# Performance work log

Hardware: AMD Instinct MI355X
Metric: run time of the kernel (lower is better)

The kernel has to match this reference:

```python
import jax, jax.numpy as jnp
import numpy as np
from jax import lax

B = 8192
H = 64      # hidden_size
O = 3       # output_size (== LSTM input size)
L = 2       # num_layers


def setup_inputs() -> dict:
    key = jax.random.key(0)
    ks = jax.random.split(key, 16)
    s = 1.0 / np.sqrt(H)
    inp = {
        "x": jax.random.normal(ks[0], (B, 1, O), dtype=jnp.float32),
        "hidden": jax.random.normal(ks[1], (L, B, H), dtype=jnp.float32),
        "cell": jax.random.normal(ks[2], (L, B, H), dtype=jnp.float32),
        # layer 0 LSTM params (PyTorch gate order i, f, g, o)
        "Wih0": jax.random.uniform(ks[3], (4 * H, O), jnp.float32, -s, s),
        "Whh0": jax.random.uniform(ks[4], (4 * H, H), jnp.float32, -s, s),
        "bih0": jax.random.uniform(ks[5], (4 * H,), jnp.float32, -s, s),
        "bhh0": jax.random.uniform(ks[6], (4 * H,), jnp.float32, -s, s),
        # layer 1 LSTM params
        "Wih1": jax.random.uniform(ks[7], (4 * H, H), jnp.float32, -s, s),
        "Whh1": jax.random.uniform(ks[8], (4 * H, H), jnp.float32, -s, s),
        "bih1": jax.random.uniform(ks[9], (4 * H,), jnp.float32, -s, s),
        "bhh1": jax.random.uniform(ks[10], (4 * H,), jnp.float32, -s, s),
        # output projection
        "Wfc": jax.random.uniform(ks[11], (O, H), jnp.float32, -s, s),
        "bfc": jax.random.uniform(ks[12], (O,), jnp.float32, -s, s),
        "num_steps": 64,
    }
    return inp


def _lstm_layer_step(x_t, h, c, Wih, Whh, b):
    # x_t: [B, in], h/c: [B, H]; gates in PyTorch order i, f, g, o
    gates = x_t @ Wih.T + h @ Whh.T + b  # [B, 4H]
    i, f, g, o = jnp.split(gates, 4, axis=-1)
    c_new = jax.nn.sigmoid(f) * c + jax.nn.sigmoid(i) * jnp.tanh(g)
    h_new = jax.nn.sigmoid(o) * jnp.tanh(c_new)
    return h_new, c_new


def reference(x, hidden, cell, Wih0, Whh0, bih0, bhh0,
              Wih1, Whh1, bih1, bhh1, Wfc, bfc, num_steps):
    layers = ((Wih0, Whh0, bih0 + bhh0), (Wih1, Whh1, bih1 + bhh1))

    def step(carry, _):
        inp, h, c = carry  # inp: [B, O], h/c: [L, B, H]
        x_t = inp
        hs, cs = [], []
        for l, (Wih, Whh, b) in enumerate(layers):
            h_l, c_l = _lstm_layer_step(x_t, h[l], c[l], Wih, Whh, b)
            hs.append(h_l)
            cs.append(c_l)
            x_t = h_l
        out = x_t @ Wfc.T + bfc  # [B, O] -> fed back as next input
        return (out, jnp.stack(hs), jnp.stack(cs)), out

    init = (x[:, 0, :], hidden, cell)
    _, outs = lax.scan(step, init, None, length=num_steps)  # [T, B, O]
    return jnp.transpose(outs, (1, 0, 2))  # [B, T, O]
```

## Files before the change

kernel.cpp:

```cpp
#include <hip/hip_runtime.h>

typedef __attribute__((ext_vector_type(8))) short v8s;
typedef __attribute__((ext_vector_type(4))) float v4f;

#define NB 16
#define TMAX 64
#define B_TOT 8192

#define BL0_U 0
#define BL1_U 32768
#define BFC_U 98304
#define NUSH  100352
#define B0_F  50176
#define B1_F  50432
#define BFC3_F 50688

__device__ __forceinline__ unsigned short f2bh(float f) {
    unsigned u = __float_as_uint(f);
    return (unsigned short)((u + 0x7fffu + ((u >> 16) & 1u)) >> 16);
}
__device__ __forceinline__ float bh2f(unsigned short h) {
    return __uint_as_float(((unsigned)h) << 16);
}
__device__ __forceinline__ float sigm(float x) {
    return 1.f / (1.f + __expf(-x));
}
__device__ __forceinline__ float tanh_(float x) {
    float e = __expf(-2.f * fabsf(x));
    float r = (1.f - e) / (1.f + e);
    return copysignf(r, x);
}
__device__ __forceinline__ v8s ldfrag(const unsigned short* p) { return *(const v8s*)p; }

#define MFMA(a, b, c) __builtin_amdgcn_mfma_f32_16x16x32_bf16((a), (b), (c), 0, 0, 0)

__global__ void repack(const float* __restrict__ Whh0,
                       const float* __restrict__ bih0, const float* __restrict__ bhh0,
                       const float* __restrict__ Wih1, const float* __restrict__ Whh1,
                       const float* __restrict__ bih1, const float* __restrict__ bhh1,
                       const float* __restrict__ Wfc,  const float* __restrict__ bfc,
                       float* __restrict__ wsf) {
    unsigned idx = blockIdx.x * 256 + threadIdx.x;
    unsigned short* wsu = (unsigned short*)wsf;
    if (idx < NUSH) {
        unsigned u, fid, l, e, s, kst, n, r, k;
        float wv;
        if (idx < BL1_U) {
            u = idx; fid = u >> 9; l = (u >> 3) & 63; e = u & 7;
            s = fid & 1; unsigned t = fid >> 1; kst = t & 1; n = t >> 1;
            r = n * 16 + (l & 15); k = kst * 32 + ((l >> 4) * 8) + e;
            wv = Whh0[r * 64 + k];
        } else if (idx < BFC_U) {
            u = idx - BL1_U; fid = u >> 9; l = (u >> 3) & 63; e = u & 7;
            s = fid & 1; unsigned t = fid >> 1; kst = t & 3; n = t >> 2;
            r = n * 16 + (l & 15); k = kst * 32 + ((l >> 4) * 8) + e;
            wv = (k < 64) ? Wih1[r * 64 + k] : Whh1[r * 64 + (k - 64)];
        } else {
            u = idx - BFC_U; fid = u >> 9; l = (u >> 3) & 63; e = u & 7;
            s = fid & 1; kst = fid >> 1;
            unsigned o = l & 15; k = kst * 32 + ((l >> 4) * 8) + e;
            wv = (o < 3) ? Wfc[o * 64 + k] : 0.f;
        }
        unsigned short hi = f2bh(wv);
        wsu[idx] = s ? f2bh(wv - bh2f(hi)) : hi;
    } else {
        unsigned jj = idx - NUSH;
        if (jj < 256) wsf[B0_F + jj] = bih0[jj] + bhh0[jj];
        else if (jj < 512) wsf[B1_F + (jj - 256)] = bih1[jj - 256] + bhh1[jj - 256];
        else if (jj < 515) wsf[BFC3_F + (jj - 512)] = bfc[jj - 512];
    }
}

__global__ __launch_bounds__(256, 2) void lstm_main(
    const float* __restrict__ x0, const float* __restrict__ h_init,
    const float* __restrict__ c_init, const float* __restrict__ Wih0,
    const float* __restrict__ wsf, const int* __restrict__ nsp,
    float* __restrict__ out)
{
    __shared__ __align__(16) unsigned short Th0[2][2][2][512];
    __shared__ __align__(16) unsigned short Th1[2][2][2][512];
    __shared__ __align__(16) float xs[2][NB][4];
    __shared__ __align__(16) float obuf[NB][TMAX * 3];

    const unsigned short* wsu = (const unsigned short*)wsf;
    const int tid = threadIdx.x, l = tid & 63, w = tid >> 6;
    const int b0g = blockIdx.x * NB;
    const int n = nsp[0];
    const int j = w * 16 + (l & 15);
    const int jh = j >> 5, kl = j & 31;
    const int bfirst = (l >> 4) * 4;
    const int stoff = ((kl >> 3) * 128) + (kl & 7) + bfirst * 8;

    v8s bl0h[4][2], bl1h[4][4];
#pragma unroll
    for (int g = 0; g < 4; ++g) {
        const int n_ = 4 * g + w;
#pragma unroll
        for (int k = 0; k < 2; ++k)
            bl0h[g][k] = ldfrag(wsu + BL0_U + ((n_ * 2 + k) * 2 + 0) * 512 + l * 8);
#pragma unroll
        for (int k = 0; k < 4; ++k)
            bl1h[g][k] = ldfrag(wsu + BL1_U + ((n_ * 4 + k) * 2 + 0) * 512 + l * 8);
    }
    float bias0[4], bias1[4], wx[4][3];
#pragma unroll
    for (int g = 0; g < 4; ++g) {
        bias0[g] = wsf[B0_F + g * 64 + j];
        bias1[g] = wsf[B1_F + g * 64 + j];
#pragma unroll
        for (int oi = 0; oi < 3; ++oi) wx[g][oi] = Wih0[(g * 64 + j) * 3 + oi];
    }
    const float mybfc = ((l & 15) < 3) ? wsf[BFC3_F + (l & 15)] : 0.f;

    float c0[4], c1[4];
#pragma unroll
    for (int r = 0; r < 4; ++r) {
        const int b = bfirst + r, bg = b0g + b;
        c0[r] = c_init[bg * 64 + j];
        c1[r] = c_init[B_TOT * 64 + bg * 64 + j];
        float h0v = h_init[bg * 64 + j];
        float h1v = h_init[B_TOT * 64 + bg * 64 + j];
        unsigned short hh = f2bh(h0v);
        Th0[0][0][jh][stoff + r * 8] = hh;
        Th0[0][1][jh][stoff + r * 8] = f2bh(h0v - bh2f(hh));
        hh = f2bh(h1v);
        Th1[0][0][jh][stoff + r * 8] = hh;
        Th1[0][1][jh][stoff + r * 8] = f2bh(h1v - bh2f(hh));
    }
    if (tid < NB * 3) {
        int b = tid / 3, o = tid % 3;
        xs[0][b][o] = x0[(b0g + b) * 3 + o];
    }
    __syncthreads();

    int cur = 0;
    for (int t = 0; t < n; ++t) {
        const int nxt = cur ^ 1;
        v8s bl0l[4][2];
#pragma unroll
        for (int g = 0; g < 4; ++g)
#pragma unroll
            for (int k = 0; k < 2; ++k)
                bl0l[g][k] = ldfrag(wsu + BL0_U + (((4 * g + w) * 2 + k) * 2 + 1) * 512 + l * 8);

        v4f acc[4];
#pragma unroll
        for (int g = 0; g < 4; ++g) acc[g] = (v4f){bias0[g], bias0[g], bias0[g], bias0[g]};

#pragma unroll
        for (int r = 0; r < 4; ++r) {
            float4 xv = *(const float4*)&xs[cur][bfirst + r][0];
#pragma unroll
            for (int g = 0; g < 4; ++g)
                acc[g][r] += wx[g][0] * xv.x + wx[g][1] * xv.y + wx[g][2] * xv.z;
        }
#pragma unroll
        for (int k = 0; k < 2; ++k) {
            v8s ah = *(const v8s*)&Th0[cur][0][k][l * 8];
            v8s al = *(const v8s*)&Th0[cur][1][k][l * 8];
#pragma unroll
            for (int g = 0; g < 4; ++g) acc[g] = MFMA(ah, bl0h[g][k], acc[g]);
#pragma unroll
            for (int g = 0; g < 4; ++g) acc[g] = MFMA(al, bl0h[g][k], acc[g]);
#pragma unroll
            for (int g = 0; g < 4; ++g) acc[g] = MFMA(ah, bl0l[g][k], acc[g]);
        }
#pragma unroll
        for (int r = 0; r < 4; ++r) {
            float ig = sigm(acc[0][r]), fg = sigm(acc[1][r]);
            float gg = tanh_(acc[2][r]), og = sigm(acc[3][r]);
            float cn = fg * c0[r] + ig * gg;
            c0[r] = cn;
            float h = og * tanh_(cn);
            unsigned short hh = f2bh(h);
            Th0[nxt][0][jh][stoff + r * 8] = hh;
            Th0[nxt][1][jh][stoff + r * 8] = f2bh(h - bh2f(hh));
        }
        v8s bl1l[4][4];
#pragma unroll
        for (int g = 0; g < 4; ++g)
#pragma unroll
            for (int k = 0; k < 4; ++k)
                bl1l[g][k] = ldfrag(wsu + BL1_U + (((4 * g + w) * 4 + k) * 2 + 1) * 512 + l * 8);

        __syncthreads();

#pragma unroll
        for (int g = 0; g < 4; ++g) acc[g] = (v4f){bias1[g], bias1[g], bias1[g], bias1[g]};
#pragma unroll
        for (int k = 0; k < 4; ++k) {
            v8s ah, al;
            if (k < 2) { ah = *(const v8s*)&Th0[nxt][0][k][l * 8];
                         al = *(const v8s*)&Th0[nxt][1][k][l * 8]; }
            else       { ah = *(const v8s*)&Th1[cur][0][k - 2][l * 8];
                         al = *(const v8s*)&Th1[cur][1][k - 2][l * 8]; }
#pragma unroll
            for (int g = 0; g < 4; ++g) acc[g] = MFMA(ah, bl1h[g][k], acc[g]);
#pragma unroll
            for (int g = 0; g < 4; ++g) acc[g] = MFMA(al, bl1h[g][k], acc[g]);
#pragma unroll
            for (int g = 0; g < 4; ++g) acc[g] = MFMA(ah, bl1l[g][k], acc[g]);
        }
#pragma unroll
        for (int r = 0; r < 4; ++r) {
            float ig = sigm(acc[0][r]), fg = sigm(acc[1][r]);
            float gg = tanh_(acc[2][r]), og = sigm(acc[3][r]);
            float cn = fg * c1[r] + ig * gg;
            c1[r] = cn;
            float h = og * tanh_(cn);
            unsigned short hh = f2bh(h);
            Th1[nxt][0][jh][stoff + r * 8] = hh;
            Th1[nxt][1][jh][stoff + r * 8] = f2bh(h - bh2f(hh));
        }
        __syncthreads();

        if (w == 0) {
            v8s bfh[2], bfl[2];
#pragma unroll
            for (int k = 0; k < 2; ++k) {
                bfh[k] = ldfrag(wsu + BFC_U + (k * 2 + 0) * 512 + l * 8);
                bfl[k] = ldfrag(wsu + BFC_U + (k * 2 + 1) * 512 + l * 8);
            }
            v4f af = (v4f){mybfc, mybfc, mybfc, mybfc};
#pragma unroll
            for (int k = 0; k < 2; ++k) {
                v8s ah = *(const v8s*)&Th1[nxt][0][k][l * 8];
                v8s al = *(const v8s*)&Th1[nxt][1][k][l * 8];
                af = MFMA(ah, bfh[k], af);
                af = MFMA(al, bfh[k], af);
                af = MFMA(ah, bfl[k], af);
            }
            if ((l & 15) < 3) {
                const int o = l & 15;
#pragma unroll
                for (int r = 0; r < 4; ++r) {
                    const int b = bfirst + r;
                    float v = af[r];
                    obuf[b][t * 3 + o] = v;
                    xs[nxt][b][o] = v;
                }
            }
        }
        __syncthreads();
        cur = nxt;
    }

    const int tot = NB * n * 3;
    for (int i = tid; i < tot; i += 256) {
        int b = i / (n * 3), r2 = i % (n * 3);
        out[(b0g + b) * (n * 3) + r2] = obuf[b][r2];
    }
}

extern "C" void kernel_launch(void* const* d_in, const int* in_sizes, int n_in,
                              void* d_out, int out_size, void* d_ws, size_t ws_size,
                              hipStream_t stream) {
    const float* x    = (const float*)d_in[0];
    const float* hid  = (const float*)d_in[1];
    const float* cel  = (const float*)d_in[2];
    const float* Wih0 = (const float*)d_in[3];
    const float* Whh0 = (const float*)d_in[4];
    const float* bih0 = (const float*)d_in[5];
    const float* bhh0 = (const float*)d_in[6];
    const float* Wih1 = (const float*)d_in[7];
    const float* Whh1 = (const float*)d_in[8];
    const float* bih1 = (const float*)d_in[9];
    const float* bhh1 = (const float*)d_in[10];
    const float* Wfc  = (const float*)d_in[11];
    const float* bfc  = (const float*)d_in[12];
    const int*   nst  = (const int*)d_in[13];
    float* ws  = (float*)d_ws;
    float* outp = (float*)d_out;

    const int repack_threads = NUSH + 515;
    repack<<<(repack_threads + 255) / 256, 256, 0, stream>>>(
        Whh0, bih0, bhh0, Wih1, Whh1, bih1, bhh1, Wfc, bfc, ws);
    lstm_main<<<B_TOT / NB, 256, 0, stream>>>(x, hid, cel, Wih0, ws, nst, outp);
}
```

Baseline: 399.6 us.

## Split gate columns across 8 waves with LDS gate exchange for activations

```diff
diff --git a/kernel.cpp b/kernel.cpp
--- a/kernel.cpp
+++ b/kernel.cpp
@@ -6,6 +6,7 @@
 #define NB 16
 #define TMAX 64
 #define B_TOT 8192
+#define GP 21
 
 #define BL0_U 0
 #define BL1_U 32768
@@ -71,7 +72,8 @@
     }
 }
 
-__global__ __launch_bounds__(256, 2) void lstm_main(
+__global__ __launch_bounds__(512) __attribute__((amdgpu_waves_per_eu(4)))
+void lstm_main(
     const float* __restrict__ x0, const float* __restrict__ h_init,
     const float* __restrict__ c_init, const float* __restrict__ Wih0,
     const float* __restrict__ wsf, const int* __restrict__ nsp,
@@ -79,6 +81,7 @@
 {
     __shared__ __align__(16) unsigned short Th0[2][2][2][512];
     __shared__ __align__(16) unsigned short Th1[2][2][2][512];
+    __shared__ float gbuf[256][GP];
     __shared__ __align__(16) float xs[2][NB][4];
     __shared__ __align__(16) float obuf[NB][TMAX * 3];
 
@@ -86,46 +89,51 @@
     const int tid = threadIdx.x, l = tid & 63, w = tid >> 6;
     const int b0g = blockIdx.x * NB;
     const int n = nsp[0];
-    const int j = w * 16 + (l & 15);
-    const int jh = j >> 5, kl = j & 31;
+    const int n0 = 2 * w;
+    const int colA = n0 * 16 + (l & 15);
     const int bfirst = (l >> 4) * 4;
-    const int stoff = ((kl >> 3) * 128) + (kl & 7) + bfirst * 8;
-
-    v8s bl0h[4][2], bl1h[4][4];
-#pragma unroll
-    for (int g = 0; g < 4; ++g) {
-        const int n_ = 4 * g + w;
-#pragma unroll
-        for (int k = 0; k < 2; ++k)
-            bl0h[g][k] = ldfrag(wsu + BL0_U + ((n_ * 2 + k) * 2 + 0) * 512 + l * 8);
-#pragma unroll
-        for (int k = 0; k < 4; ++k)
-            bl1h[g][k] = ldfrag(wsu + BL1_U + ((n_ * 4 + k) * 2 + 0) * 512 + l * 8);
-    }
-    float bias0[4], bias1[4], wx[4][3];
-#pragma unroll
-    for (int g = 0; g < 4; ++g) {
-        bias0[g] = wsf[B0_F + g * 64 + j];
-        bias1[g] = wsf[B1_F + g * 64 + j];
-#pragma unroll
-        for (int oi = 0; oi < 3; ++oi) wx[g][oi] = Wih0[(g * 64 + j) * 3 + oi];
+    const int ab = tid >> 5;
+    const int aj0 = (tid & 31) << 1;
+
+    v8s b0h[2][2], b1hA[2][2];
+#pragma unroll
+    for (int nt = 0; nt < 2; ++nt) {
+#pragma unroll
+        for (int k = 0; k < 2; ++k) {
+            b0h[nt][k]  = ldfrag(wsu + BL0_U + ((((n0 + nt) * 2 + k) * 2 + 0) << 9) + (l << 3));
+            b1hA[nt][k] = ldfrag(wsu + BL1_U + ((((n0 + nt) * 4 + k) * 2 + 0) << 9) + (l << 3));
+        }
+    }
+    float bias0[2], bias1[2], wx[2][3];
+#pragma unroll
+    for (int nt = 0; nt < 2; ++nt) {
+        const int cc = colA + nt * 16;
+        bias0[nt] = wsf[B0_F + cc];
+        bias1[nt] = wsf[B1_F + cc];
+#pragma unroll
+        for (int oi = 0; oi < 3; ++oi) wx[nt][oi] = Wih0[cc * 3 + oi];
     }
     const float mybfc = ((l & 15) < 3) ? wsf[BFC3_F + (l & 15)] : 0.f;
 
-    float c0[4], c1[4];
-#pragma unroll
-    for (int r = 0; r < 4; ++r) {
-        const int b = bfirst + r, bg = b0g + b;
-        c0[r] = c_init[bg * 64 + j];
-        c1[r] = c_init[B_TOT * 64 + bg * 64 + j];
-        float h0v = h_init[bg * 64 + j];
-        float h1v = h_init[B_TOT * 64 + bg * 64 + j];
-        unsigned short hh = f2bh(h0v);
-        Th0[0][0][jh][stoff + r * 8] = hh;
-        Th0[0][1][jh][stoff + r * 8] = f2bh(h0v - bh2f(hh));
-        hh = f2bh(h1v);
-        Th1[0][0][jh][stoff + r * 8] = hh;
-        Th1[0][1][jh][stoff + r * 8] = f2bh(h1v - bh2f(hh));
+    float c0[2], c1[2];
+    {
+        const int bg = b0g + ab;
+#pragma unroll
+        for (int m = 0; m < 2; ++m) {
+            const int jj = aj0 + m;
+            c0[m] = c_init[bg * 64 + jj];
+            c1[m] = c_init[B_TOT * 64 + bg * 64 + jj];
+            float h0v = h_init[bg * 64 + jj];
+            float h1v = h_init[B_TOT * 64 + bg * 64 + jj];
+            const int jh = jj >> 5, kl = jj & 31;
+            const int idx = ((kl >> 3) << 7) + (ab << 3) + (kl & 7);
+            unsigned short hh = f2bh(h0v);
+            Th0[0][0][jh][idx] = hh;
+            Th0[0][1][jh][idx] = f2bh(h0v - bh2f(hh));
+            hh = f2bh(h1v);
+            Th1[0][0][jh][idx] = hh;
+            Th1[0][1][jh][idx] = f2bh(h1v - bh2f(hh));
+        }
     }
     if (tid < NB * 3) {
         int b = tid / 3, o = tid % 3;
@@ -136,91 +144,164 @@
     int cur = 0;
     for (int t = 0; t < n; ++t) {
         const int nxt = cur ^ 1;
-        v8s bl0l[4][2];
-#pragma unroll
-        for (int g = 0; g < 4; ++g)
+        v8s b0l[2][2];
+#pragma unroll
+        for (int nt = 0; nt < 2; ++nt)
 #pragma unroll
             for (int k = 0; k < 2; ++k)
-                bl0l[g][k] = ldfrag(wsu + BL0_U + (((4 * g + w) * 2 + k) * 2 + 1) * 512 + l * 8);
-
-        v4f acc[4];
-#pragma unroll
-        for (int g = 0; g < 4; ++g) acc[g] = (v4f){bias0[g], bias0[g], bias0[g], bias0[g]};
-
-#pragma unroll
-        for (int r = 0; r < 4; ++r) {
-            float4 xv = *(const float4*)&xs[cur][bfirst + r][0];
-#pragma unroll
-            for (int g = 0; g < 4; ++g)
-                acc[g][r] += wx[g][0] * xv.x + wx[g][1] * xv.y + wx[g][2] * xv.z;
-        }
-#pragma unroll
-        for (int k = 0; k < 2; ++k) {
-            v8s ah = *(const v8s*)&Th0[cur][0][k][l * 8];
-            v8s al = *(const v8s*)&Th0[cur][1][k][l * 8];
-#pragma unroll
-            for (int g = 0; g < 4; ++g) acc[g] = MFMA(ah, bl0h[g][k], acc[g]);
-#pragma unroll
-            for (int g = 0; g < 4; ++g) acc[g] = MFMA(al, bl0h[g][k], acc[g]);
-#pragma unroll
-            for (int g = 0; g < 4; ++g) acc[g] = MFMA(ah, bl0l[g][k], acc[g]);
-        }
-#pragma unroll
-        for (int r = 0; r < 4; ++r) {
-            float ig = sigm(acc[0][r]), fg = sigm(acc[1][r]);
-            float gg = tanh_(acc[2][r]), og = sigm(acc[3][r]);
-            float cn = fg * c0[r] + ig * gg;
-            c0[r] = cn;
+                b0l[nt][k] = ldfrag(wsu + BL0_U + ((((n0 + nt) * 2 + k) * 2 + 1) << 9) + (l << 3));
+
+        {
+            v4f acc[2];
+#pragma unroll
+            for (int nt = 0; nt < 2; ++nt)
+                acc[nt] = (v4f){bias0[nt], bias0[nt], bias0[nt], bias0[nt]};
+#pragma unroll
+            for (int r = 0; r < 4; ++r) {
+                float4 xv = *(const float4*)&xs[cur][bfirst + r][0];
+#pragma unroll
+                for (int nt = 0; nt < 2; ++nt)
+                    acc[nt][r] += wx[nt][0] * xv.x + wx[nt][1] * xv.y + wx[nt][2] * xv.z;
+            }
+#pragma unroll
+            for (int k = 0; k < 2; ++k) {
+                v8s ah = *(const v8s*)&Th0[cur][0][k][l * 8];
+                v8s al = *(const v8s*)&Th0[cur][1][k][l * 8];
+#pragma unroll
+                for (int nt = 0; nt < 2; ++nt) {
+                    acc[nt] = MFMA(ah, b0h[nt][k], acc[nt]);
+                    acc[nt] = MFMA(al, b0h[nt][k], acc[nt]);
+                    acc[nt] = MFMA(ah, b0l[nt][k], acc[nt]);
+                }
+            }
+#pragma unroll
+            for (int nt = 0; nt < 2; ++nt) {
+                const int cc = colA + nt * 16;
+#pragma unroll
+                for (int r = 0; r < 4; ++r) gbuf[cc][bfirst + r] = acc[nt][r];
+            }
+        }
+        __syncthreads();
+
+        v8s l01[2][2];
+#pragma unroll
+        for (int nt = 0; nt < 2; ++nt)
+#pragma unroll
+            for (int k = 0; k < 2; ++k)
+                l01[nt][k] = ldfrag(wsu + BL1_U + ((((n0 + nt) * 4 + k) * 2 + 1) << 9) + (l << 3));
+
+#pragma unroll
+        for (int m = 0; m < 2; ++m) {
+            const int jj = aj0 + m;
+            float ig = sigm(gbuf[jj][ab]);
+            float fg = sigm(gbuf[64 + jj][ab]);
+            float gg = tanh_(gbuf[128 + jj][ab]);
+            float og = sigm(gbuf[192 + jj][ab]);
+            float cn = fg * c0[m] + ig * gg;
+            c0[m] = cn;
             float h = og * tanh_(cn);
             unsigned short hh = f2bh(h);
-            Th0[nxt][0][jh][stoff + r * 8] = hh;
-            Th0[nxt][1][jh][stoff + r * 8] = f2bh(h - bh2f(hh));
-        }
-        v8s bl1l[4][4];
-#pragma unroll
-        for (int g = 0; g < 4; ++g)
-#pragma unroll
-            for (int k = 0; k < 4; ++k)
-                bl1l[g][k] = ldfrag(wsu + BL1_U + (((4 * g + w) * 4 + k) * 2 + 1) * 512 + l * 8);
-
-        __syncthreads();
-
-#pragma unroll
-        for (int g = 0; g < 4; ++g) acc[g] = (v4f){bias1[g], bias1[g], bias1[g], bias1[g]};
-#pragma unroll
-        for (int k = 0; k < 4; ++k) {
-            v8s ah, al;
-            if (k < 2) { ah = *(const v8s*)&Th0[nxt][0][k][l * 8];
-                         al = *(const v8s*)&Th0[nxt][1][k][l * 8]; }
-            else       { ah = *(const v8s*)&Th1[cur][0][k - 2][l * 8];
-                         al = *(const v8s*)&Th1[cur][1][k - 2][l * 8]; }
-#pragma unroll
-            for (int g = 0; g < 4; ++g) acc[g] = MFMA(ah, bl1h[g][k], acc[g]);
-#pragma unroll
-            for (int g = 0; g < 4; ++g) acc[g] = MFMA(al, bl1h[g][k], acc[g]);
-#pragma unroll
-            for (int g = 0; g < 4; ++g) acc[g] = MFMA(ah, bl1l[g][k], acc[g]);
-        }
-#pragma unroll
-        for (int r = 0; r < 4; ++r) {
-            float ig = sigm(acc[0][r]), fg = sigm(acc[1][r]);
-            float gg = tanh_(acc[2][r]), og = sigm(acc[3][r]);
-            float cn = fg * c1[r] + ig * gg;
-            c1[r] = cn;
+            const int jh = jj >> 5, kl = jj & 31;
+            const int idx = ((kl >> 3) << 7) + (ab << 3) + (kl & 7);
+            Th0[nxt][0][jh][idx] = hh;
+            Th0[nxt][1][jh][idx] = f2bh(h - bh2f(hh));
+        }
+        __syncthreads();
+
+        {
+            v4f acc[2];
+#pragma unroll
+            for (int nt = 0; nt < 2; ++nt)
+                acc[nt] = (v4f){bias1[nt], bias1[nt], bias1[nt], bias1[nt]};
+
+            v8s h2[2], l2[2];
+#pragma unroll
+            for (int nt = 0; nt < 2; ++nt) {
+                h2[nt] = ldfrag(wsu + BL1_U + ((((n0 + nt) * 4 + 2) * 2 + 0) << 9) + (l << 3));
+                l2[nt] = ldfrag(wsu + BL1_U + ((((n0 + nt) * 4 + 2) * 2 + 1) << 9) + (l << 3));
+            }
+            {
+                v8s ah = *(const v8s*)&Th0[nxt][0][0][l * 8];
+                v8s al = *(const v8s*)&Th0[nxt][1][0][l * 8];
+#pragma unroll
+                for (int nt = 0; nt < 2; ++nt) {
+                    acc[nt] = MFMA(ah, b1hA[nt][0], acc[nt]);
+                    acc[nt] = MFMA(al, b1hA[nt][0], acc[nt]);
+                    acc[nt] = MFMA(ah, l01[nt][0], acc[nt]);
+                }
+            }
+            v8s h3[2], l3[2];
+#pragma unroll
+            for (int nt = 0; nt < 2; ++nt) {
+                h3[nt] = ldfrag(wsu + BL1_U + ((((n0 + nt) * 4 + 3) * 2 + 0) << 9) + (l << 3));
+                l3[nt] = ldfrag(wsu + BL1_U + ((((n0 + nt) * 4 + 3) * 2 + 1) << 9) + (l << 3));
+            }
+            {
+                v8s ah = *(const v8s*)&Th0[nxt][0][1][l * 8];
+                v8s al = *(const v8s*)&Th0[nxt][1][1][l * 8];
+#pragma unroll
+                for (int nt = 0; nt < 2; ++nt) {
+                    acc[nt] = MFMA(ah, b1hA[nt][1], acc[nt]);
+                    acc[nt] = MFMA(al, b1hA[nt][1], acc[nt]);
+                    acc[nt] = MFMA(ah, l01[nt][1], acc[nt]);
+                }
+            }
+            {
+                v8s ah = *(const v8s*)&Th1[cur][0][0][l * 8];
+                v8s al = *(const v8s*)&Th1[cur][1][0][l * 8];
+#pragma unroll
+                for (int nt = 0; nt < 2; ++nt) {
+                    acc[nt] = MFMA(ah, h2[nt], acc[nt]);
+                    acc[nt] = MFMA(al, h2[nt], acc[nt]);
+                    acc[nt] = MFMA(ah, l2[nt], acc[nt]);
+                }
+            }
+            {
+                v8s ah = *(const v8s*)&Th1[cur][0][1][l * 8];
+                v8s al = *(const v8s*)&Th1[cur][1][1][l * 8];
+#pragma unroll
+                for (int nt = 0; nt < 2; ++nt) {
+                    acc[nt] = MFMA(ah, h3[nt], acc[nt]);
+                    acc[nt] = MFMA(al, h3[nt], acc[nt]);
+                    acc[nt] = MFMA(ah, l3[nt], acc[nt]);
+                }
+            }
+#pragma unroll
+            for (int nt = 0; nt < 2; ++nt) {
+                const int cc = colA + nt * 16;
+#pragma unroll
+                for (int r = 0; r < 4; ++r) gbuf[cc][bfirst + r] = acc[nt][r];
+            }
+        }
+        __syncthreads();
+
+        v8s bfh[2], bfl[2];
+        if (w == 0) {
+#pragma unroll
+            for (int k = 0; k < 2; ++k) {
+                bfh[k] = ldfrag(wsu + BFC_U + (((k) * 2 + 0) << 9) + (l << 3));
+                bfl[k] = ldfrag(wsu + BFC_U + (((k) * 2 + 1) << 9) + (l << 3));
+            }
+        }
+#pragma unroll
+        for (int m = 0; m < 2; ++m) {
+            const int jj = aj0 + m;
+            float ig = sigm(gbuf[jj][ab]);
+            float fg = sigm(gbuf[64 + jj][ab]);
+            float gg = tanh_(gbuf[128 + jj][ab]);
+            float og = sigm(gbuf[192 + jj][ab]);
+            float cn = fg * c1[m] + ig * gg;
+            c1[m] = cn;
             float h = og * tanh_(cn);
             unsigned short hh = f2bh(h);
-            Th1[nxt][0][jh][stoff + r * 8] = hh;
-            Th1[nxt][1][jh][stoff + r * 8] = f2bh(h - bh2f(hh));
+            const int jh = jj >> 5, kl = jj & 31;
+            const int idx = ((kl >> 3) << 7) + (ab << 3) + (kl & 7);
+            Th1[nxt][0][jh][idx] = hh;
+            Th1[nxt][1][jh][idx] = f2bh(h - bh2f(hh));
         }
         __syncthreads();
 
         if (w == 0) {
-            v8s bfh[2], bfl[2];
-#pragma unroll
-            for (int k = 0; k < 2; ++k) {
-                bfh[k] = ldfrag(wsu + BFC_U + (k * 2 + 0) * 512 + l * 8);
-                bfl[k] = ldfrag(wsu + BFC_U + (k * 2 + 1) * 512 + l * 8);
-            }
             v4f af = (v4f){mybfc, mybfc, mybfc, mybfc};
 #pragma unroll
             for (int k = 0; k < 2; ++k) {
@@ -246,7 +327,7 @@
     }
 
     const int tot = NB * n * 3;
-    for (int i = tid; i < tot; i += 256) {
+    for (int i = tid; i < tot; i += 512) {
         int b = i / (n * 3), r2 = i % (n * 3);
         out[(b0g + b) * (n * 3) + r2] = obuf[b][r2];
     }
@@ -275,5 +356,5 @@
     const int repack_threads = NUSH + 515;
     repack<<<(repack_threads + 255) / 256, 256, 0, stream>>>(
         Whh0, bih0, bhh0, Wih1, Whh1, bih1, bhh1, Wfc, bfc, ws);
-    lstm_main<<<B_TOT / NB, 256, 0, stream>>>(x, hid, cel, Wih0, ws, nst, outp);
-}
+    lstm_main<<<B_TOT / NB, 512, 0, stream>>>(x, hid, cel, Wih0, ws, nst, outp);
+}
```

Measured after the change: 697.8 us. +74.6%, slower.

## Switch LSTM recurrence to single fp16 MFMA and drop output LDS staging

Applied to the files above, without the earlier changes.

```diff
diff --git a/kernel.cpp b/kernel.cpp
--- a/kernel.cpp
+++ b/kernel.cpp
@@ -1,27 +1,19 @@
 #include <hip/hip_runtime.h>
 
-typedef __attribute__((ext_vector_type(8))) short v8s;
+typedef __attribute__((ext_vector_type(8))) _Float16 v8h;
 typedef __attribute__((ext_vector_type(4))) float v4f;
 
-#define NB 16
-#define TMAX 64
+#define MB 16
 #define B_TOT 8192
 
-#define BL0_U 0
-#define BL1_U 32768
-#define BFC_U 98304
-#define NUSH  100352
-#define B0_F  50176
-#define B1_F  50432
-#define BFC3_F 50688
-
-__device__ __forceinline__ unsigned short f2bh(float f) {
-    unsigned u = __float_as_uint(f);
-    return (unsigned short)((u + 0x7fffu + ((u >> 16) & 1u)) >> 16);
-}
-__device__ __forceinline__ float bh2f(unsigned short h) {
-    return __uint_as_float(((unsigned)h) << 16);
-}
+#define L0_H 0
+#define L1_H 16384
+#define FC_H 49152
+#define NHALF 50176
+#define B0_F 25088
+#define B1_F 25344
+#define BFC3_F 25600
+
 __device__ __forceinline__ float sigm(float x) {
     return 1.f / (1.f + __expf(-x));
 }
@@ -30,9 +22,8 @@
     float r = (1.f - e) / (1.f + e);
     return copysignf(r, x);
 }
-__device__ __forceinline__ v8s ldfrag(const unsigned short* p) { return *(const v8s*)p; }
-
-#define MFMA(a, b, c) __builtin_amdgcn_mfma_f32_16x16x32_bf16((a), (b), (c), 0, 0, 0)
+
+#define MFMAH(a, b, c) __builtin_amdgcn_mfma_f32_16x16x32_f16((a), (b), (c), 0, 0, 0)
 
 __global__ void repack(const float* __restrict__ Whh0,
                        const float* __restrict__ bih0, const float* __restrict__ bhh0,
@@ -41,214 +32,178 @@
                        const float* __restrict__ Wfc,  const float* __restrict__ bfc,
                        float* __restrict__ wsf) {
     unsigned idx = blockIdx.x * 256 + threadIdx.x;
-    unsigned short* wsu = (unsigned short*)wsf;
-    if (idx < NUSH) {
-        unsigned u, fid, l, e, s, kst, n, r, k;
+    _Float16* wsh = (_Float16*)wsf;
+    if (idx < NHALF) {
+        unsigned l = (idx >> 3) & 63, e = idx & 7;
         float wv;
-        if (idx < BL1_U) {
-            u = idx; fid = u >> 9; l = (u >> 3) & 63; e = u & 7;
-            s = fid & 1; unsigned t = fid >> 1; kst = t & 1; n = t >> 1;
-            r = n * 16 + (l & 15); k = kst * 32 + ((l >> 4) * 8) + e;
+        if (idx < L1_H) {
+            unsigned fid = idx >> 9, nt = fid >> 1, kst = fid & 1;
+            unsigned r = nt * 16 + (l & 15), k = kst * 32 + ((l >> 4) << 3) + e;
             wv = Whh0[r * 64 + k];
-        } else if (idx < BFC_U) {
-            u = idx - BL1_U; fid = u >> 9; l = (u >> 3) & 63; e = u & 7;
-            s = fid & 1; unsigned t = fid >> 1; kst = t & 3; n = t >> 2;
-            r = n * 16 + (l & 15); k = kst * 32 + ((l >> 4) * 8) + e;
+        } else if (idx < FC_H) {
+            unsigned u = idx - L1_H, fid = u >> 9, nt = fid >> 2, kst = fid & 3;
+            unsigned r = nt * 16 + (l & 15), k = kst * 32 + ((l >> 4) << 3) + e;
             wv = (k < 64) ? Wih1[r * 64 + k] : Whh1[r * 64 + (k - 64)];
         } else {
-            u = idx - BFC_U; fid = u >> 9; l = (u >> 3) & 63; e = u & 7;
-            s = fid & 1; kst = fid >> 1;
-            unsigned o = l & 15; k = kst * 32 + ((l >> 4) * 8) + e;
+            unsigned u = idx - FC_H, kst = u >> 9;
+            unsigned o = l & 15, k = kst * 32 + ((l >> 4) << 3) + e;
             wv = (o < 3) ? Wfc[o * 64 + k] : 0.f;
         }
-        unsigned short hi = f2bh(wv);
-        wsu[idx] = s ? f2bh(wv - bh2f(hi)) : hi;
+        wsh[idx] = (_Float16)wv;
     } else {
-        unsigned jj = idx - NUSH;
+        unsigned jj = idx - NHALF;
         if (jj < 256) wsf[B0_F + jj] = bih0[jj] + bhh0[jj];
         else if (jj < 512) wsf[B1_F + (jj - 256)] = bih1[jj - 256] + bhh1[jj - 256];
         else if (jj < 515) wsf[BFC3_F + (jj - 512)] = bfc[jj - 512];
     }
 }
 
-__global__ __launch_bounds__(256, 2) void lstm_main(
+__global__ __launch_bounds__(256)
+void lstm_main(
     const float* __restrict__ x0, const float* __restrict__ h_init,
     const float* __restrict__ c_init, const float* __restrict__ Wih0,
     const float* __restrict__ wsf, const int* __restrict__ nsp,
     float* __restrict__ out)
 {
-    __shared__ __align__(16) unsigned short Th0[2][2][2][512];
-    __shared__ __align__(16) unsigned short Th1[2][2][2][512];
-    __shared__ __align__(16) float xs[2][NB][4];
-    __shared__ __align__(16) float obuf[NB][TMAX * 3];
-
-    const unsigned short* wsu = (const unsigned short*)wsf;
+    __shared__ _Float16 Th0[2][2][512];
+    __shared__ _Float16 Th1[2][2][512];
+
+    const _Float16* wsh = (const _Float16*)wsf;
     const int tid = threadIdx.x, l = tid & 63, w = tid >> 6;
-    const int b0g = blockIdx.x * NB;
+    const int b0g = blockIdx.x * MB;
     const int n = nsp[0];
-    const int j = w * 16 + (l & 15);
-    const int jh = j >> 5, kl = j & 31;
+    const int c15 = l & 15;
     const int bfirst = (l >> 4) * 4;
-    const int stoff = ((kl >> 3) * 128) + (kl & 7) + bfirst * 8;
-
-    v8s bl0h[4][2], bl1h[4][4];
+    const int j = 16 * w + c15;
+    const int kh = j >> 5, kl = j & 31;
+    const int hwoff = ((kl >> 3) << 7) + (bfirst << 3) + (kl & 7);
+    const int sbase = l & 48;
+
+    v8h wb0[4][2], wb1[4][4], wfc2[2];
 #pragma unroll
     for (int g = 0; g < 4; ++g) {
-        const int n_ = 4 * g + w;
+        const int nt = 4 * g + w;
 #pragma unroll
         for (int k = 0; k < 2; ++k)
-            bl0h[g][k] = ldfrag(wsu + BL0_U + ((n_ * 2 + k) * 2 + 0) * 512 + l * 8);
+            wb0[g][k] = *(const v8h*)(wsh + L0_H + ((nt * 2 + k) << 9) + (l << 3));
 #pragma unroll
         for (int k = 0; k < 4; ++k)
-            bl1h[g][k] = ldfrag(wsu + BL1_U + ((n_ * 4 + k) * 2 + 0) * 512 + l * 8);
-    }
-    float bias0[4], bias1[4], wx[4][3];
+            wb1[g][k] = *(const v8h*)(wsh + L1_H + ((nt * 4 + k) << 9) + (l << 3));
+    }
+#pragma unroll
+    for (int k = 0; k < 2; ++k)
+        wfc2[k] = *(const v8h*)(wsh + FC_H + (k << 9) + (l << 3));
+
+    float bias0[4], bias1[4];
+    v8h wxp0 = {}, wxp1 = {};
 #pragma unroll
     for (int g = 0; g < 4; ++g) {
-        bias0[g] = wsf[B0_F + g * 64 + j];
-        bias1[g] = wsf[B1_F + g * 64 + j];
-#pragma unroll
-        for (int oi = 0; oi < 3; ++oi) wx[g][oi] = Wih0[(g * 64 + j) * 3 + oi];
-    }
-    const float mybfc = ((l & 15) < 3) ? wsf[BFC3_F + (l & 15)] : 0.f;
+        const int cc = 64 * g + j;
+        bias0[g] = wsf[B0_F + cc];
+        bias1[g] = wsf[B1_F + cc];
+#pragma unroll
+        for (int o = 0; o < 3; ++o) {
+            const int ii = g * 3 + o;
+            _Float16 v = (_Float16)Wih0[cc * 3 + o];
+            if (ii < 8) wxp0[ii] = v; else wxp1[ii - 8] = v;
+        }
+    }
+    const float mybfc = (c15 < 3) ? wsf[BFC3_F + c15] : 0.f;
 
     float c0[4], c1[4];
-#pragma unroll
-    for (int r = 0; r < 4; ++r) {
-        const int b = bfirst + r, bg = b0g + b;
-        c0[r] = c_init[bg * 64 + j];
-        c1[r] = c_init[B_TOT * 64 + bg * 64 + j];
-        float h0v = h_init[bg * 64 + j];
-        float h1v = h_init[B_TOT * 64 + bg * 64 + j];
-        unsigned short hh = f2bh(h0v);
-        Th0[0][0][jh][stoff + r * 8] = hh;
-        Th0[0][1][jh][stoff + r * 8] = f2bh(h0v - bh2f(hh));
-        hh = f2bh(h1v);
-        Th1[0][0][jh][stoff + r * 8] = hh;
-        Th1[0][1][jh][stoff + r * 8] = f2bh(h1v - bh2f(hh));
-    }
-    if (tid < NB * 3) {
-        int b = tid / 3, o = tid % 3;
-        xs[0][b][o] = x0[(b0g + b) * 3 + o];
+    v4f af;
+    int ob[4];
+    {
+        const int n3 = n * 3;
+#pragma unroll
+        for (int r = 0; r < 4; ++r) {
+            const int bg = b0g + bfirst + r;
+            c0[r] = c_init[bg * 64 + j];
+            c1[r] = c_init[B_TOT * 64 + bg * 64 + j];
+            Th0[0][kh][hwoff + r * 8] = (_Float16)h_init[bg * 64 + j];
+            Th1[0][kh][hwoff + r * 8] = (_Float16)h_init[B_TOT * 64 + bg * 64 + j];
+            af[r] = (c15 < 3) ? x0[bg * 3 + c15] : 0.f;
+            ob[r] = bg * n3 + c15;
+        }
     }
     __syncthreads();
 
     int cur = 0;
     for (int t = 0; t < n; ++t) {
         const int nxt = cur ^ 1;
-        v8s bl0l[4][2];
-#pragma unroll
-        for (int g = 0; g < 4; ++g)
-#pragma unroll
-            for (int k = 0; k < 2; ++k)
-                bl0l[g][k] = ldfrag(wsu + BL0_U + (((4 * g + w) * 2 + k) * 2 + 1) * 512 + l * 8);
-
-        v4f acc[4];
-#pragma unroll
-        for (int g = 0; g < 4; ++g) acc[g] = (v4f){bias0[g], bias0[g], bias0[g], bias0[g]};
-
-#pragma unroll
-        for (int r = 0; r < 4; ++r) {
-            float4 xv = *(const float4*)&xs[cur][bfirst + r][0];
+        {
+            v4f acc[4];
 #pragma unroll
             for (int g = 0; g < 4; ++g)
-                acc[g][r] += wx[g][0] * xv.x + wx[g][1] * xv.y + wx[g][2] * xv.z;
-        }
-#pragma unroll
-        for (int k = 0; k < 2; ++k) {
-            v8s ah = *(const v8s*)&Th0[cur][0][k][l * 8];
-            v8s al = *(const v8s*)&Th0[cur][1][k][l * 8];
-#pragma unroll
-            for (int g = 0; g < 4; ++g) acc[g] = MFMA(ah, bl0h[g][k], acc[g]);
-#pragma unroll
-            for (int g = 0; g < 4; ++g) acc[g] = MFMA(al, bl0h[g][k], acc[g]);
-#pragma unroll
-            for (int g = 0; g < 4; ++g) acc[g] = MFMA(ah, bl0l[g][k], acc[g]);
-        }
-#pragma unroll
-        for (int r = 0; r < 4; ++r) {
-            float ig = sigm(acc[0][r]), fg = sigm(acc[1][r]);
-            float gg = tanh_(acc[2][r]), og = sigm(acc[3][r]);
-            float cn = fg * c0[r] + ig * gg;
-            c0[r] = cn;
-            float h = og * tanh_(cn);
-            unsigned short hh = f2bh(h);
-            Th0[nxt][0][jh][stoff + r * 8] = hh;
-            Th0[nxt][1][jh][stoff + r * 8] = f2bh(h - bh2f(hh));
-        }
-        v8s bl1l[4][4];
-#pragma unroll
-        for (int g = 0; g < 4; ++g)
-#pragma unroll
-            for (int k = 0; k < 4; ++k)
-                bl1l[g][k] = ldfrag(wsu + BL1_U + (((4 * g + w) * 4 + k) * 2 + 1) * 512 + l * 8);
-
+                acc[g] = (v4f){bias0[g], bias0[g], bias0[g], bias0[g]};
+#pragma unroll
+            for (int r = 0; r < 4; ++r) {
+#pragma unroll
+                for (int o = 0; o < 3; ++o) {
+                    float xv = __shfl(af[r], sbase | o);
+#pragma unroll
+                    for (int g = 0; g < 4; ++g) {
+                        const int ii = g * 3 + o;
+                        float wgt = (ii < 8) ? (float)wxp0[ii] : (float)wxp1[ii - 8];
+                        acc[g][r] += wgt * xv;
+                    }
+                }
+            }
+#pragma unroll
+            for (int k = 0; k < 2; ++k) {
+                v8h ah = *(const v8h*)&Th0[cur][k][l * 8];
+#pragma unroll
+                for (int g = 0; g < 4; ++g) acc[g] = MFMAH(ah, wb0[g][k], acc[g]);
+            }
+#pragma unroll
+            for (int r = 0; r < 4; ++r) {
+                float ig = sigm(acc[0][r]), fg = sigm(acc[1][r]);
+                float gg = tanh_(acc[2][r]), og = sigm(acc[3][r]);
+                float cn = fg * c0[r] + ig * gg;
+                c0[r] = cn;
+                Th0[nxt][kh][hwoff + r * 8] = (_Float16)(og * tanh_(cn));
+            }
+        }
         __syncthreads();
 
-#pragma unroll
-        for (int g = 0; g < 4; ++g) acc[g] = (v4f){bias1[g], bias1[g], bias1[g], bias1[g]};
-#pragma unroll
-        for (int k = 0; k < 4; ++k) {
-            v8s ah, al;
-            if (k < 2) { ah = *(const v8s*)&Th0[nxt][0][k][l * 8];
-                         al = *(const v8s*)&Th0[nxt][1][k][l * 8]; }
-            else       { ah = *(const v8s*)&Th1[cur][0][k - 2][l * 8];
-                         al = *(const v8s*)&Th1[cur][1][k - 2][l * 8]; }
-#pragma unroll
-            for (int g = 0; g < 4; ++g) acc[g] = MFMA(ah, bl1h[g][k], acc[g]);
-#pragma unroll
-            for (int g = 0; g < 4; ++g) acc[g] = MFMA(al, bl1h[g][k], acc[g]);
-#pragma unroll
-            for (int g = 0; g < 4; ++g) acc[g] = MFMA(ah, bl1l[g][k], acc[g]);
-        }
-#pragma unroll
-        for (int r = 0; r < 4; ++r) {
-            float ig = sigm(acc[0][r]), fg = sigm(acc[1][r]);
-            float gg = tanh_(acc[2][r]), og = sigm(acc[3][r]);
-            float cn = fg * c1[r] + ig * gg;
-            c1[r] = cn;
-            float h = og * tanh_(cn);
-            unsigned short hh = f2bh(h);
-            Th1[nxt][0][jh][stoff + r * 8] = hh;
-            Th1[nxt][1][jh][stoff + r * 8] = f2bh(h - bh2f(hh));
+        {
+            v4f acc[4];
+#pragma unroll
+            for (int g = 0; g < 4; ++g)
+                acc[g] = (v4f){bias1[g], bias1[g], bias1[g], bias1[g]};
+#pragma unroll
+            for (int k = 0; k < 4; ++k) {
+                v8h ah = (k < 2) ? *(const v8h*)&Th0[nxt][k][l * 8]
+                                 : *(const v8h*)&Th1[cur][k - 2][l * 8];
+#pragma unroll
+                for (int g = 0; g < 4; ++g) acc[g] = MFMAH(ah, wb1[g][k], acc[g]);
+            }
+#pragma unroll
+            for (int r = 0; r < 4; ++r) {
+                float ig = sigm(acc[0][r]), fg = sigm(acc[1][r]);
+                float gg = tanh_(acc[2][r]), og = sigm(acc[3][r]);
+                float cn = fg * c1[r] + ig * gg;
+                c1[r] = cn;
+                Th1[nxt][kh][hwoff + r * 8] = (_Float16)(og * tanh_(cn));
+            }
         }
         __syncthreads();
 
-        if (w == 0) {
-            v8s bfh[2], bfl[2];
+        {
+            v4f afv = (v4f){mybfc, mybfc, mybfc, mybfc};
 #pragma unroll
             for (int k = 0; k < 2; ++k) {
-                bfh[k] = ldfrag(wsu + BFC_U + (k * 2 + 0) * 512 + l * 8);
-                bfl[k] = ldfrag(wsu + BFC_U + (k * 2 + 1) * 512 + l * 8);
-            }
-            v4f af = (v4f){mybfc, mybfc, mybfc, mybfc};
-#pragma unroll
-            for (int k = 0; k < 2; ++k) {
-                v8s ah = *(const v8s*)&Th1[nxt][0][k][l * 8];
-                v8s al = *(const v8s*)&Th1[nxt][1][k][l * 8];
-                af = MFMA(ah, bfh[k], af);
-                af = MFMA(al, bfh[k], af);
-                af = MFMA(ah, bfl[k], af);
-            }
-            if ((l & 15) < 3) {
-                const int o = l & 15;
-#pragma unroll
-                for (int r = 0; r < 4; ++r) {
-                    const int b = bfirst + r;
-                    float v = af[r];
-                    obuf[b][t * 3 + o] = v;
-                    xs[nxt][b][o] = v;
-                }
-            }
-        }
-        __syncthreads();
+                v8h ah = *(const v8h*)&Th1[nxt][k][l * 8];
+                afv = MFMAH(ah, wfc2[k], afv);
+            }
+            af = afv;
+            if (w == 0 && c15 < 3) {
+#pragma unroll
+                for (int r = 0; r < 4; ++r)
+                    out[ob[r] + t * 3] = afv[r];
+            }
+        }
         cur = nxt;
-    }
-
-    const int tot = NB * n * 3;
-    for (int i = tid; i < tot; i += 256) {
-        int b = i / (n * 3), r2 = i % (n * 3);
-        out[(b0g + b) * (n * 3) + r2] = obuf[b][r2];
     }
 }
 
@@ -272,8 +227,8 @@
     float* ws  = (float*)d_ws;
     float* outp = (float*)d_out;
 
-    const int repack_threads = NUSH + 515;
+    const int repack_threads = NHALF + 515;
     repack<<<(repack_threads + 255) / 256, 256, 0, stream>>>(
         Whh0, bih0, bhh0, Wih1, Whh1, bih1, bhh1, Wfc, bfc, ws);
-    lstm_main<<<B_TOT / NB, 256, 0, stream>>>(x, hid, cel, Wih0, ws, nst, outp);
-}
+    lstm_main<<<B_TOT / MB, 256, 0, stream>>>(x, hid, cel, Wih0, ws, nst, outp);
+}
```

After: 352.9 us. -11.7%, faster.
